# Performance work log

Measured on AMD Instinct MI355X. Metric: run time of the kernel, lower is better.

## Reference

```python
import jax, jax.numpy as jnp
import numpy as np
import math

N = 20000          # real nodes (batch_size)
D = 256            # hidden_dim
H = 4              # num_heads
L = 3              # num_layers
E = 320000         # local edges
EXP_DEG = 4        # expander_degree
LN_EPS = 1e-5


def setup_inputs() -> dict:
    key = jax.random.key(0)
    ks = jax.random.split(key, 8)
    x = jax.random.normal(ks[0], (N, D), jnp.float32)
    rng = np.random.default_rng(0)
    edge_index = jnp.asarray(rng.integers(0, N, size=(2, E)), dtype=jnp.int32)
    # Expander: EXP_DEG//2 random permutations on N+1 nodes (incl. virtual node),
    # each contributing edges in both directions -> degree-EXP_DEG regular graph.
    n = N + 1
    perms = [rng.permutation(n) for _ in range(EXP_DEG // 2)]
    src = np.concatenate([np.arange(n) for _ in perms] + perms)
    dst = np.concatenate(perms + [np.arange(n) for _ in perms])
    exp_edge_index = jnp.asarray(np.stack([src, dst]), dtype=jnp.int32)
    s_in = 1.0 / math.sqrt(D)
    s_ffn = 1.0 / math.sqrt(4 * D)
    def w(k, shape, s):
        return jax.random.normal(k, shape, jnp.float32) * s
    params = {
        'Wqkv_loc': w(ks[1], (L, D, 3 * D), s_in), 'bqkv_loc': jnp.zeros((L, 3 * D), jnp.float32),
        'Wo_loc':   w(ks[2], (L, D, D), s_in),     'bo_loc':   jnp.zeros((L, D), jnp.float32),
        'Wqkv_exp': w(ks[3], (L, D, 3 * D), s_in), 'bqkv_exp': jnp.zeros((L, 3 * D), jnp.float32),
        'Wo_exp':   w(ks[4], (L, D, D), s_in),     'bo_exp':   jnp.zeros((L, D), jnp.float32),
        'ln_g': jnp.ones((L, D), jnp.float32),     'ln_b': jnp.zeros((L, D), jnp.float32),
        'W1': w(ks[5], (L, D, 4 * D), s_in),       'b1': jnp.zeros((L, 4 * D), jnp.float32),
        'W2': w(ks[6], (L, 4 * D, D), s_ffn),      'b2': jnp.zeros((L, D), jnp.float32),
    }
    return {'x': x, 'edge_index': edge_index, 'exp_edge_index': exp_edge_index, **params}


def _attention(h, src, dst, Wqkv, bqkv, Wo, bo):
    # Sparse multi-head attention over (src -> dst) edges with segment softmax per dst.
    n, d = h.shape
    dh = d // H
    qkv = (h @ Wqkv + bqkv).reshape(n, 3, H, dh)
    q, k, v = qkv[:, 0], qkv[:, 1], qkv[:, 2]            # [n, H, dh]
    score = (q[dst] * k[src]).sum(-1) / jnp.sqrt(jnp.float32(dh))  # [e, H]
    m = jax.ops.segment_max(score, dst, num_segments=n)  # [n, H]
    ex = jnp.exp(score - m[dst])
    denom = jax.ops.segment_sum(ex, dst, num_segments=n)
    alpha = ex / (denom[dst] + 1e-16)
    out = jax.ops.segment_sum(alpha[:, :, None] * v[src], dst, num_segments=n)  # [n, H, dh]
    return out.reshape(n, d) @ Wo + bo


def _layer_norm(x, g, b):
    mu = x.mean(-1, keepdims=True)
    var = ((x - mu) ** 2).mean(-1, keepdims=True)
    return (x - mu) * jax.lax.rsqrt(var + LN_EPS) * g + b


def reference(x, edge_index, exp_edge_index, Wqkv_loc, bqkv_loc, Wo_loc, bo_loc,
              Wqkv_exp, bqkv_exp, Wo_exp, bo_exp, ln_g, ln_b, W1, b1, W2, b2):
    n0 = x.shape[0]
    # VirtualNode transform: append one zero-feature node connected to/from all nodes.
    h = jnp.concatenate([x, jnp.zeros((1, x.shape[1]), x.dtype)], axis=0)
    ar = jnp.arange(n0, dtype=edge_index.dtype)
    vn = jnp.full((n0,), n0, dtype=edge_index.dtype)
    src = jnp.concatenate([edge_index[0], ar, vn])
    dst = jnp.concatenate([edge_index[1], vn, ar])
    esrc, edst = exp_edge_index[0], exp_edge_index[1]
    for l in range(L):  # fixed small number of structurally distinct layers
        res = h
        loc = _attention(h, src, dst, Wqkv_loc[l], bqkv_loc[l], Wo_loc[l], bo_loc[l])
        exp = _attention(h, esrc, edst, Wqkv_exp[l], bqkv_exp[l], Wo_exp[l], bo_exp[l])
        h = _layer_norm(res + loc + exp, ln_g[l], ln_b[l])
        h = h + (jax.nn.gelu(h @ W1[l] + b1[l], approximate=False) @ W2[l] + b2[l])
    return h[:n0]
```

## Files before the change

kernel.cpp:

```cpp
#include <hip/hip_runtime.h>
#include <stdint.h>

#define NREAL   20000
#define NNODES  20001
#define VN      20000
#define E_EDGES 320000
#define NEXP    80004
#define MPAD    20096
#define NVNW    320

typedef unsigned short u16;
typedef unsigned int   u32;
typedef __bf16 bf16x8 __attribute__((ext_vector_type(8)));
typedef float  f32x4  __attribute__((ext_vector_type(4)));
typedef u16    u16x8  __attribute__((ext_vector_type(8)));

__device__ __host__ __forceinline__ size_t fmoff(int row, int col, int LD) {
    return (size_t)(row >> 4) * ((size_t)LD * 16) + (size_t)((col >> 3) * 128)
         + (size_t)((row & 15) * 8) + (size_t)(col & 7);
}

__device__ __forceinline__ int qkv_perm(int n) {
    if (n < 256) return n;
    int u = n - 256;
    int part = u >> 8;
    int cl = u & 255;
    return 256 + (cl >> 2) * 8 + part * 4 + (cl & 3);
}

__device__ __forceinline__ float bf2f(u16 v) {
    union { u32 u; float f; } x; x.u = ((u32)v) << 16; return x.f;
}
__device__ __forceinline__ u16 f2bf(float f) {
    union { float f; u32 u; } x; x.f = f;
    u32 r = (x.u + 0x7fffu + ((x.u >> 16) & 1u)) >> 16;
    return (u16)r;
}
__device__ __forceinline__ float4 cvt4(ushort4 u) {
    return make_float4(bf2f(u.x), bf2f(u.y), bf2f(u.z), bf2f(u.w));
}
__device__ __forceinline__ float4 ld4bf(const u16* p) { return cvt4(*(const ushort4*)p); }
__device__ __forceinline__ float4 cvtk8(u16x8 r) {
    return make_float4(bf2f(r[0]), bf2f(r[1]), bf2f(r[2]), bf2f(r[3]));
}
__device__ __forceinline__ float4 cvtv8(u16x8 r) {
    return make_float4(bf2f(r[4]), bf2f(r[5]), bf2f(r[6]), bf2f(r[7]));
}


__global__ void hinit_kernel(const float* __restrict__ x, float* __restrict__ h,
                             u16* __restrict__ hb) {
    int idx = blockIdx.x * 256 + threadIdx.x;
    if (idx >= NNODES * 64) return;
    int row = idx >> 6, c0 = (idx & 63) * 4;
    float4 v = make_float4(0.f, 0.f, 0.f, 0.f);
    if (row < NREAL) v = *(const float4*)(x + (size_t)row * 256 + c0);
    *(float4*)(h + (size_t)row * 256 + c0) = v;
    ushort4 o;
    o.x = f2bf(v.x); o.y = f2bf(v.y); o.z = f2bf(v.z); o.w = f2bf(v.w);
    *(ushort4*)(hb + fmoff(row, c0, 256)) = o;
}

__global__ void init_kernel(int* cnt, int* fill, int* ecnt,
                            const float* __restrict__ bl, const float* __restrict__ be,
                            float* __restrict__ bcat,
                            const float* __restrict__ bol, const float* __restrict__ boe,
                            float* __restrict__ bsum) {
    int i = blockIdx.x * 256 + threadIdx.x;
    if (i < NREAL) { cnt[i] = 0; fill[i] = 0; }
    if (i < NNODES) ecnt[i] = 0;
    if (i < 3 * 1536) {
        int l = i / 1536, c = i - l * 1536;
        float v = (c < 768) ? bl[l * 768 + c] : be[l * 768 + c - 768];
        int cc = (c >= 768) ? c - 768 : c;
        int d = qkv_perm(cc) + ((c >= 768) ? 768 : 0);
        bcat[l * 1536 + d] = v;
    }
    if (i < 3 * 256) bsum[i] = bol[i] + boe[i];
}

__global__ void csr_count_kernel(const int* __restrict__ ei, int* __restrict__ cnt) {
    int e = blockIdx.x * 256 + threadIdx.x;
    if (e < E_EDGES) atomicAdd(&cnt[ei[E_EDGES + e]], 1);
}

__global__ void csr_scan_kernel(const int* __restrict__ cnt, int* __restrict__ indptr) {
    __shared__ int ssum[256];
    int t = threadIdx.x;
    int c0 = t * 79;
    int s = 0;
    for (int j = 0; j < 79; j++) {
        int i = c0 + j;
        if (i < NREAL) s += cnt[i];
    }
    ssum[t] = s;
    __syncthreads();
    for (int d2 = 1; d2 < 256; d2 <<= 1) {
        int v = (t >= d2) ? ssum[t - d2] : 0;
        __syncthreads();
        ssum[t] += v;
        __syncthreads();
    }
    int run = (t == 0) ? 0 : ssum[t - 1];
    for (int j = 0; j < 79; j++) {
        int i = c0 + j;
        if (i < NREAL) { indptr[i] = run; run += cnt[i]; }
    }
    if (t == 255) indptr[NREAL] = run;
}

__global__ void csr_scatter_kernel(const int* __restrict__ ei, const int* __restrict__ indptr,
                                   int* __restrict__ fill, int* __restrict__ srcs) {
    int e = blockIdx.x * 256 + threadIdx.x;
    if (e < E_EDGES) {
        int d = ei[E_EDGES + e];
        int pos = indptr[d] + atomicAdd(&fill[d], 1);
        srcs[pos] = ei[e];
    }
}

__global__ void exp_scatter_kernel(const int* __restrict__ eei, int* __restrict__ ecnt,
                                   int* __restrict__ esrcs) {
    int e = blockIdx.x * 256 + threadIdx.x;
    if (e < NEXP) {
        int d = eei[NEXP + e];
        int pos = atomicAdd(&ecnt[d], 1);
        esrcs[d * 4 + pos] = eei[e];
    }
}

__global__ void wconv_all_kernel(const float* __restrict__ WqkvL, const float* __restrict__ WqkvE,
                                 const float* __restrict__ WoL, const float* __restrict__ WoE,
                                 const float* __restrict__ W1, const float* __restrict__ W2,
                                 u16* __restrict__ out) {
    int i = blockIdx.x * 256 + threadIdx.x;
    if (i >= 3 * 1048576) return;
    int l = i / 1048576, r = i - l * 1048576;
    if (r >= 393216 && r < 524288) {
        int r2 = r - 393216;
        int k = r2 >> 8, n = r2 & 255;
        float v = (k < 256) ? WoL[(size_t)l * 65536 + k * 256 + n]
                            : WoE[(size_t)l * 65536 + (k - 256) * 256 + n];
        out[(size_t)l * 1048576 + 393216 + fmoff(n, k, 512)] = f2bf(v);
        return;
    }
    const float* src; int K, N; int base;
    if (r < 196608)      { src = WqkvL; K = 256;  N = 768;  base = 0; }
    else if (r < 393216) { src = WqkvE; K = 256;  N = 768;  base = 196608; }
    else if (r < 786432) { src = W1;    K = 256;  N = 1024; base = 524288; }
    else                 { src = W2;    K = 1024; N = 256;  base = 786432; }
    int r2 = r - base;
    int k = r2 / N, n = r2 - k * N;
    int d = (r < 393216) ? qkv_perm(n) : n;
    out[(size_t)l * 1048576 + base + fmoff(d, k, K)] = f2bf(src[(size_t)l * K * N + r2]);
}

__global__ __launch_bounds__(256) void qkv_rw(
    const u16* __restrict__ A, const u16* __restrict__ Bt, const float* __restrict__ bias,
    u16* __restrict__ Q0, u16* __restrict__ KV0,
    u16* __restrict__ Q1, u16* __restrict__ KV1, int M) {
    const int lin = blockIdx.x;
    const int mt = lin / 6, ns = lin - mt * 6;
    const int tm = mt * 32;
    if (tm >= M) return;
    const int tid = threadIdx.x;
    const int w = tid >> 6, lane = tid & 63;
    const int lm = lane & 15, q = lane >> 4;

    f32x4 acc[2][4];
#pragma unroll
    for (int a = 0; a < 2; a++)
#pragma unroll
        for (int b = 0; b < 4; b++) acc[a][b] = (f32x4)0.0f;

    const u16* apf[2];
    const u16* bpf[4];
#pragma unroll
    for (int mi = 0; mi < 2; mi++)
        apf[mi] = A + (size_t)(tm / 16 + mi) * 4096 + q * 128 + lm * 8;
#pragma unroll
    for (int ni = 0; ni < 4; ni++)
        bpf[ni] = Bt + (size_t)(ns * 16 + w * 4 + ni) * 4096 + q * 128 + lm * 8;

    bf16x8 sA[4][2], sB[4][4];
#pragma unroll
    for (int s = 0; s < 3; s++) {
#pragma unroll
        for (int mi = 0; mi < 2; mi++) sA[s][mi] = *(const bf16x8*)(apf[mi] + s * 512);
#pragma unroll
        for (int ni = 0; ni < 4; ni++) sB[s][ni] = *(const bf16x8*)(bpf[ni] + s * 512);
    }
#pragma unroll
    for (int i = 0; i < 8; i++) {
        const int cu = i & 3, pf = (i + 3) & 3;
        if (i + 3 < 8) {
#pragma unroll
            for (int mi = 0; mi < 2; mi++) sA[pf][mi] = *(const bf16x8*)(apf[mi] + (i + 3) * 512);
#pragma unroll
            for (int ni = 0; ni < 4; ni++) sB[pf][ni] = *(const bf16x8*)(bpf[ni] + (i + 3) * 512);
        }
#pragma unroll
        for (int mi = 0; mi < 2; mi++)
#pragma unroll
            for (int ni = 0; ni < 4; ni++)
                acc[mi][ni] = __builtin_amdgcn_mfma_f32_16x16x32_bf16(
                    sB[cu][ni], sA[cu][mi], acc[mi][ni], 0, 0, 0);
    }

    float4 b4[4];
#pragma unroll
    for (int ni = 0; ni < 4; ni++)
        b4[ni] = *(const float4*)(bias + ns * 256 + w * 64 + ni * 16 + q * 4);

#pragma unroll
    for (int mi = 0; mi < 2; mi++) {
        int grow = tm + mi * 16 + lm;
        if (grow >= M) continue;
#pragma unroll
        for (int ni = 0; ni < 4; ni++) {
            int gcol = ns * 256 + w * 64 + ni * 16 + q * 4;
            float v0 = acc[mi][ni][0] + b4[ni].x;
            float v1 = acc[mi][ni][1] + b4[ni].y;
            float v2 = acc[mi][ni][2] + b4[ni].z;
            float v3 = acc[mi][ni][3] + b4[ni].w;
            ushort4 o;
            o.x = f2bf(v0); o.y = f2bf(v1); o.z = f2bf(v2); o.w = f2bf(v3);
            u16* dst;
            if (gcol < 256)       dst = Q0  + (size_t)grow * 256 + gcol;
            else if (gcol < 768)  dst = KV0 + (size_t)grow * 512 + (gcol - 256);
            else if (gcol < 1024) dst = Q1  + (size_t)grow * 256 + (gcol - 768);
            else                  dst = KV1 + (size_t)grow * 512 + (gcol - 1024);
            *(ushort4*)dst = o;
        }
    }
}

__global__ __launch_bounds__(256) void ffn1_rw(
    const u16* __restrict__ A, const u16* __restrict__ Bt, const float* __restrict__ bias,
    u16* __restrict__ Cb, int M) {
    const int lin = blockIdx.x;
    const int mt = lin >> 2, ns = lin & 3;
    const int tm = mt * 32;
    if (tm >= M) return;
    const int tid = threadIdx.x;
    const int w = tid >> 6, lane = tid & 63;
    const int lm = lane & 15, q = lane >> 4;

    f32x4 acc[2][4];
#pragma unroll
    for (int a = 0; a < 2; a++)
#pragma unroll
        for (int b = 0; b < 4; b++) acc[a][b] = (f32x4)0.0f;

    const u16* apf[2];
    const u16* bpf[4];
#pragma unroll
    for (int mi = 0; mi < 2; mi++)
        apf[mi] = A + (size_t)(tm / 16 + mi) * 4096 + q * 128 + lm * 8;
#pragma unroll
    for (int ni = 0; ni < 4; ni++)
        bpf[ni] = Bt + (size_t)(ns * 16 + w * 4 + ni) * 4096 + q * 128 + lm * 8;

    bf16x8 sA[4][2], sB[4][4];
#pragma unroll
    for (int s = 0; s < 3; s++) {
#pragma unroll
        for (int mi = 0; mi < 2; mi++) sA[s][mi] = *(const bf16x8*)(apf[mi] + s * 512);
#pragma unroll
        for (int ni = 0; ni < 4; ni++) sB[s][ni] = *(const bf16x8*)(bpf[ni] + s * 512);
    }
#pragma unroll
    for (int i = 0; i < 8; i++) {
        const int cu = i & 3, pf = (i + 3) & 3;
        if (i + 3 < 8) {
#pragma unroll
            for (int mi = 0; mi < 2; mi++) sA[pf][mi] = *(const bf16x8*)(apf[mi] + (i + 3) * 512);
#pragma unroll
            for (int ni = 0; ni < 4; ni++) sB[pf][ni] = *(const bf16x8*)(bpf[ni] + (i + 3) * 512);
        }
#pragma unroll
        for (int mi = 0; mi < 2; mi++)
#pragma unroll
            for (int ni = 0; ni < 4; ni++)
                acc[mi][ni] = __builtin_amdgcn_mfma_f32_16x16x32_bf16(
                    sB[cu][ni], sA[cu][mi], acc[mi][ni], 0, 0, 0);
    }

    float4 b4[4];
#pragma unroll
    for (int ni = 0; ni < 4; ni++)
        b4[ni] = *(const float4*)(bias + ns * 256 + w * 64 + ni * 16 + q * 4);

#pragma unroll
    for (int mi = 0; mi < 2; mi++) {
        int grow = tm + mi * 16 + lm;
        if (grow >= M) continue;
#pragma unroll
        for (int ni = 0; ni < 4; ni++) {
            int gcol = ns * 256 + w * 64 + ni * 16 + q * 4;
            float v0 = acc[mi][ni][0] + b4[ni].x;
            float v1 = acc[mi][ni][1] + b4[ni].y;
            float v2 = acc[mi][ni][2] + b4[ni].z;
            float v3 = acc[mi][ni][3] + b4[ni].w;
            float g0, g1, g2, g3;
            {
                float u = 0.7978845608f * (v0 + 0.044715f * v0 * v0 * v0);
                g0 = 0.5f * v0 * (2.0f - 2.0f / (__expf(2.0f * u) + 1.0f));
            }
            {
                float u = 0.7978845608f * (v1 + 0.044715f * v1 * v1 * v1);
                g1 = 0.5f * v1 * (2.0f - 2.0f / (__expf(2.0f * u) + 1.0f));
            }
            {
                float u = 0.7978845608f * (v2 + 0.044715f * v2 * v2 * v2);
                g2 = 0.5f * v2 * (2.0f - 2.0f / (__expf(2.0f * u) + 1.0f));
            }
            {
                float u = 0.7978845608f * (v3 + 0.044715f * v3 * v3 * v3);
                g3 = 0.5f * v3 * (2.0f - 2.0f / (__expf(2.0f * u) + 1.0f));
            }
            ushort4 o;
            o.x = f2bf(g0); o.y = f2bf(g1); o.z = f2bf(g2); o.w = f2bf(g3);
            *(ushort4*)(Cb + fmoff(grow, gcol, 1024)) = o;
        }
    }
}

__global__ __launch_bounds__(256) void wo_ln_rw(
    const u16* A, const u16* __restrict__ Bt, const float* __restrict__ bias,
    const float* __restrict__ resid, const float* __restrict__ g,
    const float* __restrict__ bvec, float* __restrict__ hout, u16* __restrict__ hb,
    const float* __restrict__ part, u16* acat_w, int M) {
    __shared__ float smS[32][4];
    __shared__ float smQ[32][4];
    const int tm = blockIdx.x * 32;
    if (tm >= M) return;
    const int tid = threadIdx.x;
    const int w = tid >> 6, lane = tid & 63;
    const int lm = lane & 15, q = lane >> 4;

    if (blockIdx.x == VN / 32) {
        __shared__ float smm[4][64][6];
        int hh = lane >> 4;
        int ov = (hh << 6) + (lane & 15) * 4;
        float mm = -1e30f, ll = 0.0f;
        float ax = 0, ay = 0, az = 0, aw = 0;
        for (int p = w * 80; p < w * 80 + 80; p++) {
            const float* pp = part + (size_t)p * 264;
            float pm = pp[hh], pl = pp[4 + hh];
            float4 nm = *(const float4*)(pp + 8 + ov);
            float Mn = fmaxf(mm, pm);
            float s0 = __expf(mm - Mn);
            float s1 = __expf(pm - Mn);
            ax = ax * s0 + nm.x * s1;
            ay = ay * s0 + nm.y * s1;
            az = az * s0 + nm.z * s1;
            aw = aw * s0 + nm.w * s1;
            ll = ll * s0 + pl * s1;
            mm = Mn;
        }
        smm[w][lane][0] = mm; smm[w][lane][1] = ll;
        smm[w][lane][2] = ax; smm[w][lane][3] = ay;
        smm[w][lane][4] = az; smm[w][lane][5] = aw;
        __syncthreads();
        if (w == 0) {
            float M2 = -1e30f, L2 = 0.0f;
            float bx = 0, by = 0, bz = 0, bw = 0;
#pragma unroll
            for (int p = 0; p < 4; p++) {
                float pm = smm[p][lane][0], pl = smm[p][lane][1];
                float Mn = fmaxf(M2, pm);
                float s0 = __expf(M2 - Mn);
                float s1 = __expf(pm - Mn);
                bx = bx * s0 + smm[p][lane][2] * s1;
                by = by * s0 + smm[p][lane][3] * s1;
                bz = bz * s0 + smm[p][lane][4] * s1;
                bw = bw * s0 + smm[p][lane][5] * s1;
                L2 = L2 * s0 + pl * s1;
                M2 = Mn;
            }
            float inv = 1.0f / (L2 + 1e-16f);
            ushort4 o;
            o.x = f2bf(bx * inv); o.y = f2bf(by * inv);
            o.z = f2bf(bz * inv); o.w = f2bf(bw * inv);
            *(ushort4*)(acat_w + fmoff(VN, ov, 512)) = o;
        }
        __syncthreads();
    }

    f32x4 acc[2][4];
#pragma unroll
    for (int a = 0; a < 2; a++)
#pragma unroll
        for (int b = 0; b < 4; b++) acc[a][b] = (f32x4)0.0f;

    const u16* apf[2];
    const u16* bpf[4];
#pragma unroll
    for (int mi = 0; mi < 2; mi++)
        apf[mi] = A + (size_t)(tm / 16 + mi) * 8192 + q * 128 + lm * 8;
#pragma unroll
    for (int ni = 0; ni < 4; ni++)
        bpf[ni] = Bt + (size_t)(w * 4 + ni) * 8192 + q * 128 + lm * 8;

    bf16x8 sA[4][2], sB[4][4];
#pragma unroll
    for (int s = 0; s < 3; s++) {
#pragma unroll
        for (int mi = 0; mi < 2; mi++) sA[s][mi] = *(const bf16x8*)(apf[mi] + s * 512);
#pragma unroll
        for (int ni = 0; ni < 4; ni++) sB[s][ni] = *(const bf16x8*)(bpf[ni] + s * 512);
    }
#pragma unroll
    for (int i = 0; i < 16; i++) {
        const int cu = i & 3, pf = (i + 3) & 3;
        if (i + 3 < 16) {
#pragma unroll
            for (int mi = 0; mi < 2; mi++) sA[pf][mi] = *(const bf16x8*)(apf[mi] + (i + 3) * 512);
#pragma unroll
            for (int ni = 0; ni < 4; ni++) sB[pf][ni] = *(const bf16x8*)(bpf[ni] + (i + 3) * 512);
        }
#pragma unroll
        for (int mi = 0; mi < 2; mi++)
#pragma unroll
            for (int ni = 0; ni < 4; ni++)
                acc[mi][ni] = __builtin_amdgcn_mfma_f32_16x16x32_bf16(
                    sB[cu][ni], sA[cu][mi], acc[mi][ni], 0, 0, 0);
    }

    float4 b4[4];
#pragma unroll
    for (int ni = 0; ni < 4; ni++)
        b4[ni] = *(const float4*)(bias + w * 64 + ni * 16 + q * 4);
#pragma unroll
    for (int mi = 0; mi < 2; mi++) {
        int grow = tm + mi * 16 + lm;
#pragma unroll
        for (int ni = 0; ni < 4; ni++) {
            int gcol = w * 64 + ni * 16 + q * 4;
            size_t idx = (size_t)grow * 256 + gcol;
            float4 rv = *(const float4*)(resid + idx);
            acc[mi][ni][0] = rv.x + (acc[mi][ni][0] + b4[ni].x);
            acc[mi][ni][1] = rv.y + (acc[mi][ni][1] + b4[ni].y);
            acc[mi][ni][2] = rv.z + (acc[mi][ni][2] + b4[ni].z);
            acc[mi][ni][3] = rv.w + (acc[mi][ni][3] + b4[ni].w);
        }
    }

    float s1[2];
#pragma unroll
    for (int mi = 0; mi < 2; mi++) {
        float s = 0.f;
#pragma unroll
        for (int ni = 0; ni < 4; ni++)
            s += acc[mi][ni][0] + acc[mi][ni][1] + acc[mi][ni][2] + acc[mi][ni][3];
        s += __shfl_xor(s, 16); s += __shfl_xor(s, 32);
        s1[mi] = s;
    }
    if (lane < 16) {
        smS[lm][w] = s1[0];
        smS[16 + lm][w] = s1[1];
    }
    __syncthreads();
    float mu[2];
#pragma unroll
    for (int mi = 0; mi < 2; mi++) {
        int r = mi * 16 + lm;
        mu[mi] = (smS[r][0] + smS[r][1] + smS[r][2] + smS[r][3]) * (1.0f / 256.0f);
    }
    float s2[2];
#pragma unroll
    for (int mi = 0; mi < 2; mi++) {
        float s = 0.f;
#pragma unroll
        for (int ni = 0; ni < 4; ni++) {
            float d0 = acc[mi][ni][0] - mu[mi];
            float d1 = acc[mi][ni][1] - mu[mi];
            float d2 = acc[mi][ni][2] - mu[mi];
            float d3 = acc[mi][ni][3] - mu[mi];
            s += d0 * d0 + d1 * d1 + d2 * d2 + d3 * d3;
        }
        s += __shfl_xor(s, 16); s += __shfl_xor(s, 32);
        s2[mi] = s;
    }
    if (lane < 16) {
        smQ[lm][w] = s2[0];
        smQ[16 + lm][w] = s2[1];
    }
    __syncthreads();
    float rinv[2];
#pragma unroll
    for (int mi = 0; mi < 2; mi++) {
        int r = mi * 16 + lm;
        float var = (smQ[r][0] + smQ[r][1] + smQ[r][2] + smQ[r][3]) * (1.0f / 256.0f);
        rinv[mi] = 1.0f / sqrtf(var + 1e-5f);
    }
#pragma unroll
    for (int mi = 0; mi < 2; mi++) {
        int grow = tm + mi * 16 + lm;
        if (grow >= M) continue;
#pragma unroll
        for (int ni = 0; ni < 4; ni++) {
            int gcol = w * 64 + ni * 16 + q * 4;
            float4 gv = *(const float4*)(g + gcol);
            float4 bv = *(const float4*)(bvec + gcol);
            float4 y;
            y.x = (acc[mi][ni][0] - mu[mi]) * rinv[mi] * gv.x + bv.x;
            y.y = (acc[mi][ni][1] - mu[mi]) * rinv[mi] * gv.y + bv.y;
            y.z = (acc[mi][ni][2] - mu[mi]) * rinv[mi] * gv.z + bv.z;
            y.w = (acc[mi][ni][3] - mu[mi]) * rinv[mi] * gv.w + bv.w;
            *(float4*)(hout + (size_t)grow * 256 + gcol) = y;
            ushort4 o;
            o.x = f2bf(y.x); o.y = f2bf(y.y); o.z = f2bf(y.z); o.w = f2bf(y.w);
            *(ushort4*)(hb + fmoff(grow, gcol, 256)) = o;
        }
    }
}

__global__ __launch_bounds__(256) void w2_rw(
    const u16* __restrict__ A, const u16* __restrict__ Bt, const float* __restrict__ bias,
    const float* __restrict__ resid, float* __restrict__ Cf, u16* __restrict__ Cb,
    int last, int M) {
    const int tm = blockIdx.x * 32;
    if (tm >= M) return;
    const int tid = threadIdx.x;
    const int w = tid >> 6, lane = tid & 63;
    const int lm = lane & 15, q = lane >> 4;

    f32x4 acc[2][4];
#pragma unroll
    for (int a = 0; a < 2; a++)
#pragma unroll
        for (int b = 0; b < 4; b++) acc[a][b] = (f32x4)0.0f;

    const u16* apf[2];
    const u16* bpf[4];
#pragma unroll
    for (int mi = 0; mi < 2; mi++)
        apf[mi] = A + (size_t)(tm / 16 + mi) * 16384 + q * 128 + lm * 8;
#pragma unroll
    for (int ni = 0; ni < 4; ni++)
        bpf[ni] = Bt + (size_t)(w * 4 + ni) * 16384 + q * 128 + lm * 8;

    bf16x8 sA[4][2], sB[4][4];
#pragma unroll
    for (int s = 0; s < 3; s++) {
#pragma unroll
        for (int mi = 0; mi < 2; mi++) sA[s][mi] = *(const bf16x8*)(apf[mi] + s * 512);
#pragma unroll
        for (int ni = 0; ni < 4; ni++) sB[s][ni] = *(const bf16x8*)(bpf[ni] + s * 512);
    }
#pragma unroll
    for (int i = 0; i < 32; i++) {
        const int cu = i & 3, pf = (i + 3) & 3;
        if (i + 3 < 32) {
#pragma unroll
            for (int mi = 0; mi < 2; mi++) sA[pf][mi] = *(const bf16x8*)(apf[mi] + (i + 3) * 512);
#pragma unroll
            for (int ni = 0; ni < 4; ni++) sB[pf][ni] = *(const bf16x8*)(bpf[ni] + (i + 3) * 512);
        }
#pragma unroll
        for (int mi = 0; mi < 2; mi++)
#pragma unroll
            for (int ni = 0; ni < 4; ni++)
                acc[mi][ni] = __builtin_amdgcn_mfma_f32_16x16x32_bf16(
                    sB[cu][ni], sA[cu][mi], acc[mi][ni], 0, 0, 0);
    }

    float4 b4[4];
#pragma unroll
    for (int ni = 0; ni < 4; ni++)
        b4[ni] = *(const float4*)(bias + w * 64 + ni * 16 + q * 4);

#pragma unroll
    for (int mi = 0; mi < 2; mi++) {
        int grow = tm + mi * 16 + lm;
        if (grow >= (last ? NREAL : M)) continue;
#pragma unroll
        for (int ni = 0; ni < 4; ni++) {
            int gcol = w * 64 + ni * 16 + q * 4;
            float v0 = acc[mi][ni][0] + b4[ni].x;
            float v1 = acc[mi][ni][1] + b4[ni].y;
            float v2 = acc[mi][ni][2] + b4[ni].z;
            float v3 = acc[mi][ni][3] + b4[ni].w;
            size_t idx = (size_t)grow * 256 + gcol;
            float4 rv = *(const float4*)(resid + idx);
            float o0 = rv.x + v0, o1 = rv.y + v1, o2 = rv.z + v2, o3 = rv.w + v3;
            *(float4*)(Cf + idx) = make_float4(o0, o1, o2, o3);
            if (!last) {
                ushort4 o;
                o.x = f2bf(o0); o.y = f2bf(o1); o.z = f2bf(o2); o.w = f2bf(o3);
                *(ushort4*)(Cb + fmoff(grow, gcol, 256)) = o;
            }
        }
    }
}

__global__ void attn_fused_kernel(const u16* __restrict__ qb_loc, const u16* __restrict__ kv_loc,
                                  const u16* __restrict__ qb_exp, const u16* __restrict__ kv_exp,
                                  const int* __restrict__ indptr, const int* __restrict__ srcs,
                                  const int* __restrict__ esrcs,
                                  u16* __restrict__ acat, float* __restrict__ part) {
    int gw0 = (int)((blockIdx.x * (size_t)blockDim.x + threadIdx.x) >> 6);
    int gw = __builtin_amdgcn_readfirstlane(gw0);
    int lane = threadIdx.x & 63;
    int h = lane >> 4;
    int off = (h << 6) + (lane & 15) * 4;
    int coff = (off >> 2) * 8;

    if (gw < NVNW) {
        int wv = gw;
        float4 qv = ld4bf(qb_loc + (size_t)VN * 256 + off);
        float m = -1e30f, l = 0.0f;
        float ax = 0, ay = 0, az = 0, aw = 0;
        for (int i = wv; i < NREAL; i += NVNW) {
            u16x8 r = *(const u16x8*)(kv_loc + (size_t)i * 512 + coff);
            float4 k4 = cvtk8(r);
            float4 v4 = cvtv8(r);
            float s = qv.x * k4.x + qv.y * k4.y + qv.z * k4.z + qv.w * k4.w;
            s += __shfl_xor(s, 1); s += __shfl_xor(s, 2);
            s += __shfl_xor(s, 4); s += __shfl_xor(s, 8);
            float sc = s * 0.125f;
            float mn = fmaxf(m, sc);
            float fold = __expf(m - mn);
            float ee = __expf(sc - mn);
            ax = ax * fold + v4.x * ee;
            ay = ay * fold + v4.y * ee;
            az = az * fold + v4.z * ee;
            aw = aw * fold + v4.w * ee;
            l = l * fold + ee;
            m = mn;
        }
        float* pp = part + (size_t)wv * 264;
        if ((lane & 15) == 0) { pp[h] = m; pp[4 + h] = l; }
        *(float4*)(pp + 8 + off) = make_float4(ax, ay, az, aw);
        return;
    }
    gw -= NVNW;

    const u16 *qb, *kv;
    const int* sl;
    int node, beg, deg, tot, cbase;
    if (gw < NREAL) {
        node = gw; qb = qb_loc; kv = kv_loc; sl = srcs; cbase = 0;
        beg = indptr[node]; deg = indptr[node + 1] - beg; tot = deg + 1;
    } else if (gw < NREAL + NNODES) {
        node = gw - NREAL;
        qb = qb_exp; kv = kv_exp; sl = esrcs; cbase = 256;
        beg = node * 4; deg = 4; tot = 4;
    } else {
        return;
    }

    float4 qv = ld4bf(qb + (size_t)node * 256 + off);
    float m = -1e30f, l = 0.0f;
    float ax = 0, ay = 0, az = 0, aw = 0;

    if (tot <= 4) {
        u16x8 raw[4];
#pragma unroll
        for (int j = 0; j < 4; j++) {
            int s = (j < deg) ? sl[beg + j] : VN;
            raw[j] = *(const u16x8*)(kv + (size_t)s * 512 + coff);
        }
        float sc[4];
#pragma unroll
        for (int j = 0; j < 4; j++) {
            float4 k4 = cvtk8(raw[j]);
            float p = qv.x * k4.x + qv.y * k4.y + qv.z * k4.z + qv.w * k4.w;
            p += __shfl_xor(p, 1); p += __shfl_xor(p, 2);
            p += __shfl_xor(p, 4); p += __shfl_xor(p, 8);
            sc[j] = (j < tot) ? p * 0.125f : -1e30f;
        }
        float mn = fmaxf(fmaxf(sc[0], sc[1]), fmaxf(sc[2], sc[3]));
#pragma unroll
        for (int j = 0; j < 4; j++) {
            float ee = __expf(sc[j] - mn);
            float4 v4 = cvtv8(raw[j]);
            ax += v4.x * ee; ay += v4.y * ee; az += v4.z * ee; aw += v4.w * ee;
            l += ee;
        }
        m = mn;
    } else {
        const int nch = (tot + 7) >> 3;
        u16x8 rA[8], rB[8];
#pragma unroll
        for (int j = 0; j < 8; j++) {
            int s = (j < deg) ? sl[beg + j] : VN;
            rA[j] = *(const u16x8*)(kv + (size_t)s * 512 + coff);
        }
        for (int c = 0; c < nch; c++) {
            if (c + 1 < nch) {
                const int e0n = (c + 1) * 8;
#pragma unroll
                for (int j = 0; j < 8; j++) {
                    int e = e0n + j;
                    int s = (e < deg) ? sl[beg + e] : VN;
                    rB[j] = *(const u16x8*)(kv + (size_t)s * 512 + coff);
                }
            }
            const int e0 = c * 8;
            float sc[8];
#pragma unroll
            for (int j = 0; j < 8; j++) {
                float4 k4 = cvtk8(rA[j]);
                float p = qv.x * k4.x + qv.y * k4.y + qv.z * k4.z + qv.w * k4.w;
                p += __shfl_xor(p, 1); p += __shfl_xor(p, 2);
                p += __shfl_xor(p, 4); p += __shfl_xor(p, 8);
                sc[j] = (e0 + j < tot) ? p * 0.125f : -1e30f;
            }
            float cmax = fmaxf(fmaxf(fmaxf(sc[0], sc[1]), fmaxf(sc[2], sc[3])),
                               fmaxf(fmaxf(sc[4], sc[5]), fmaxf(sc[6], sc[7])));
            float mn = fmaxf(m, cmax);
            float fold = __expf(m - mn);
            ax *= fold; ay *= fold; az *= fold; aw *= fold; l *= fold;
#pragma unroll
            for (int j = 0; j < 8; j++) {
                float ee = __expf(sc[j] - mn);
                float4 v4 = cvtv8(rA[j]);
                ax += v4.x * ee; ay += v4.y * ee; az += v4.z * ee; aw += v4.w * ee;
                l += ee;
            }
            m = mn;
#pragma unroll
            for (int j = 0; j < 8; j++) rA[j] = rB[j];
        }
    }
    float inv = 1.0f / (l + 1e-16f);
    ushort4 o;
    o.x = f2bf(ax * inv); o.y = f2bf(ay * inv);
    o.z = f2bf(az * inv); o.w = f2bf(aw * inv);
    *(ushort4*)(acat + fmoff(node, cbase + off, 512)) = o;
}


extern "C" void kernel_launch(void* const* d_in, const int* in_sizes, int n_in,
                              void* d_out, int out_size, void* d_ws, size_t ws_size,
                              hipStream_t stream) {
    (void)in_sizes; (void)n_in; (void)out_size;
    const float* x        = (const float*)d_in[0];
    const int*   ei       = (const int*)d_in[1];
    const int*   eei      = (const int*)d_in[2];
    const float* Wqkv_loc = (const float*)d_in[3];
    const float* bqkv_loc = (const float*)d_in[4];
    const float* Wo_loc   = (const float*)d_in[5];
    const float* bo_loc   = (const float*)d_in[6];
    const float* Wqkv_exp = (const float*)d_in[7];
    const float* bqkv_exp = (const float*)d_in[8];
    const float* Wo_exp   = (const float*)d_in[9];
    const float* bo_exp   = (const float*)d_in[10];
    const float* ln_g     = (const float*)d_in[11];
    const float* ln_b     = (const float*)d_in[12];
    const float* W1       = (const float*)d_in[13];
    const float* b1       = (const float*)d_in[14];
    const float* W2       = (const float*)d_in[15];
    const float* b2       = (const float*)d_in[16];

    char* wsp = (char*)d_ws;
    size_t off = 0;
    auto carve = [&](size_t bytes) -> void* {
        void* p = wsp + off;
        off += (bytes + 255) & ~(size_t)255;
        return p;
    };
    float* h_f    = (float*)carve((size_t)NNODES * 256 * 4);
    u16*   h_b    = (u16*)carve((size_t)MPAD * 256 * 2);
    u16*   qb_loc = (u16*)carve((size_t)NNODES * 256 * 2);
    u16*   kv_loc = (u16*)carve((size_t)NNODES * 512 * 2);
    u16*   qb_exp = (u16*)carve((size_t)NNODES * 256 * 2);
    u16*   kv_exp = (u16*)carve((size_t)NNODES * 512 * 2);
    u16*   acat   = (u16*)carve((size_t)MPAD * 512 * 2);
    u16*   wbf    = (u16*)carve((size_t)3 * 1048576 * 2);
    float* bcat   = (float*)carve((size_t)3 * 1536 * 4);
    float* bsum   = (float*)carve((size_t)3 * 256 * 4);
    int*   cnt    = (int*)carve((size_t)NREAL * 4);
    int*   indptr = (int*)carve((size_t)(NREAL + 1) * 4);
    int*   fill   = (int*)carve((size_t)NREAL * 4);
    int*   srcs   = (int*)carve((size_t)E_EDGES * 4);
    int*   ecnt   = (int*)carve((size_t)NNODES * 4);
    int*   esrcs  = (int*)carve((size_t)NNODES * 4 * 4);
    float* part   = (float*)carve((size_t)NVNW * 264 * 4);
    u16*   mid_d  = (u16*)carve((size_t)MPAD * 1024 * 2);
    u16*   mid    = (ws_size >= off) ? mid_d : qb_loc;

    hinit_kernel<<<(NNODES * 64 + 255) / 256, 256, 0, stream>>>(x, h_f, h_b);
    init_kernel<<<(NNODES + 255) / 256, 256, 0, stream>>>(
        cnt, fill, ecnt, bqkv_loc, bqkv_exp, bcat, bo_loc, bo_exp, bsum);
    csr_count_kernel<<<(E_EDGES + 255) / 256, 256, 0, stream>>>(ei, cnt);
    csr_scan_kernel<<<1, 256, 0, stream>>>(cnt, indptr);
    csr_scatter_kernel<<<(E_EDGES + 255) / 256, 256, 0, stream>>>(ei, indptr, fill, srcs);
    exp_scatter_kernel<<<(NEXP + 255) / 256, 256, 0, stream>>>(eei, ecnt, esrcs);
    wconv_all_kernel<<<(3 * 1048576 + 255) / 256, 256, 0, stream>>>(
        Wqkv_loc, Wqkv_exp, Wo_loc, Wo_exp, W1, W2, wbf);

    const int ATTN_BLOCKS = (NVNW + NREAL + NNODES + 3) / 4;
    const int RW32_BLOCKS = MPAD / 32;
    const int QKV_BLOCKS  = RW32_BLOCKS * 6;
    const int FFN1_BLOCKS = RW32_BLOCKS * 4;

    for (int l = 0; l < 3; l++) {
        const u16* wqkvC = wbf + (size_t)l * 1048576 + 0;
        const u16* wocat = wbf + (size_t)l * 1048576 + 393216;
        const u16* w1T   = wbf + (size_t)l * 1048576 + 524288;
        const u16* w2T   = wbf + (size_t)l * 1048576 + 786432;

        qkv_rw<<<QKV_BLOCKS, 256, 0, stream>>>(
            h_b, wqkvC, bcat + l * 1536,
            qb_loc, kv_loc, qb_exp, kv_exp, NNODES);

        attn_fused_kernel<<<ATTN_BLOCKS, 256, 0, stream>>>(
            qb_loc, kv_loc, qb_exp, kv_exp, indptr, srcs, esrcs, acat, part);

        wo_ln_rw<<<RW32_BLOCKS, 256, 0, stream>>>(
            acat, wocat, bsum + l * 256, h_f,
            ln_g + l * 256, ln_b + l * 256, h_f, h_b, part, acat, NNODES);

        ffn1_rw<<<FFN1_BLOCKS, 256, 0, stream>>>(
            h_b, w1T, b1 + l * 1024, mid, NNODES);

        if (l < 2) {
            w2_rw<<<RW32_BLOCKS, 256, 0, stream>>>(
                mid, w2T, b2 + l * 256, h_f, h_f, h_b, 0, NNODES);
        } else {
            w2_rw<<<RW32_BLOCKS, 256, 0, stream>>>(
                mid, w2T, b2 + l * 256, h_f, (float*)d_out, nullptr, 1, NNODES);
        }
    }
}
```

Baseline: 766.4 us.

## Fuse FFN up-projection, GELU and down-projection into one kernel

Merges the W1+GELU kernel and the W2+residual kernel into a single kernel per 32-row tile. The 1024-wide GELU intermediate is produced in four 256-column chunks, each staged in LDS and immediately consumed by the W2 accumulation. This removes the global write and read of the bf16 intermediate buffer and one launch per layer. In exchange, the grid for the first GEMM shrinks to a quarter as many blocks, two block-wide barriers are added per chunk, and the register prefetch depth drops from three stages to two.

```diff
diff --git a/kernel.cpp b/kernel.cpp
--- a/kernel.cpp
+++ b/kernel.cpp
@@ -235,93 +235,168 @@
     }
 }
 
-__global__ __launch_bounds__(256) void ffn1_rw(
-    const u16* __restrict__ A, const u16* __restrict__ Bt, const float* __restrict__ bias,
-    u16* __restrict__ Cb, int M) {
-    const int lin = blockIdx.x;
-    const int mt = lin >> 2, ns = lin & 3;
-    const int tm = mt * 32;
+__global__ __launch_bounds__(256) void ffn_fused(
+    const u16* __restrict__ A, const u16* __restrict__ W1t, const u16* __restrict__ W2t,
+    const float* __restrict__ b1v, const float* __restrict__ b2v,
+    const float* __restrict__ resid, float* __restrict__ Cf, u16* __restrict__ Cb,
+    int last, int M) {
+    __shared__ u16 smid[32 * 256];
+    const int tm = blockIdx.x * 32;
     if (tm >= M) return;
     const int tid = threadIdx.x;
     const int w = tid >> 6, lane = tid & 63;
     const int lm = lane & 15, q = lane >> 4;
 
-    f32x4 acc[2][4];
+    f32x4 acc2[2][4];
 #pragma unroll
     for (int a = 0; a < 2; a++)
 #pragma unroll
-        for (int b = 0; b < 4; b++) acc[a][b] = (f32x4)0.0f;
+        for (int b = 0; b < 4; b++) acc2[a][b] = (f32x4)0.0f;
 
     const u16* apf[2];
-    const u16* bpf[4];
 #pragma unroll
     for (int mi = 0; mi < 2; mi++)
         apf[mi] = A + (size_t)(tm / 16 + mi) * 4096 + q * 128 + lm * 8;
+    const u16* bpf2[4];
 #pragma unroll
     for (int ni = 0; ni < 4; ni++)
-        bpf[ni] = Bt + (size_t)(ns * 16 + w * 4 + ni) * 4096 + q * 128 + lm * 8;
-
-    bf16x8 sA[4][2], sB[4][4];
-#pragma unroll
-    for (int s = 0; s < 3; s++) {
-#pragma unroll
-        for (int mi = 0; mi < 2; mi++) sA[s][mi] = *(const bf16x8*)(apf[mi] + s * 512);
-#pragma unroll
-        for (int ni = 0; ni < 4; ni++) sB[s][ni] = *(const bf16x8*)(bpf[ni] + s * 512);
-    }
-#pragma unroll
-    for (int i = 0; i < 8; i++) {
-        const int cu = i & 3, pf = (i + 3) & 3;
-        if (i + 3 < 8) {
-#pragma unroll
-            for (int mi = 0; mi < 2; mi++) sA[pf][mi] = *(const bf16x8*)(apf[mi] + (i + 3) * 512);
-#pragma unroll
-            for (int ni = 0; ni < 4; ni++) sB[pf][ni] = *(const bf16x8*)(bpf[ni] + (i + 3) * 512);
-        }
-#pragma unroll
-        for (int mi = 0; mi < 2; mi++)
-#pragma unroll
-            for (int ni = 0; ni < 4; ni++)
-                acc[mi][ni] = __builtin_amdgcn_mfma_f32_16x16x32_bf16(
-                    sB[cu][ni], sA[cu][mi], acc[mi][ni], 0, 0, 0);
-    }
-
-    float4 b4[4];
+        bpf2[ni] = W2t + (size_t)(w * 4 + ni) * 16384 + q * 128 + lm * 8;
+    const u16* alds[2];
+#pragma unroll
+    for (int mi = 0; mi < 2; mi++)
+        alds[mi] = smid + mi * 4096 + q * 128 + lm * 8;
+
+    for (int c = 0; c < 4; c++) {
+        f32x4 acc1[2][4];
+#pragma unroll
+        for (int a = 0; a < 2; a++)
+#pragma unroll
+            for (int b = 0; b < 4; b++) acc1[a][b] = (f32x4)0.0f;
+        const u16* bpf1[4];
+#pragma unroll
+        for (int ni = 0; ni < 4; ni++)
+            bpf1[ni] = W1t + (size_t)(c * 16 + w * 4 + ni) * 4096 + q * 128 + lm * 8;
+
+        {
+            bf16x8 sA[3][2], sB[3][4];
+#pragma unroll
+            for (int s = 0; s < 2; s++) {
+#pragma unroll
+                for (int mi = 0; mi < 2; mi++) sA[s][mi] = *(const bf16x8*)(apf[mi] + s * 512);
+#pragma unroll
+                for (int ni = 0; ni < 4; ni++) sB[s][ni] = *(const bf16x8*)(bpf1[ni] + s * 512);
+            }
+#pragma unroll
+            for (int i = 0; i < 8; i++) {
+                const int cu = i % 3, pf = (i + 2) % 3;
+                if (i + 2 < 8) {
+#pragma unroll
+                    for (int mi = 0; mi < 2; mi++)
+                        sA[pf][mi] = *(const bf16x8*)(apf[mi] + (i + 2) * 512);
+#pragma unroll
+                    for (int ni = 0; ni < 4; ni++)
+                        sB[pf][ni] = *(const bf16x8*)(bpf1[ni] + (i + 2) * 512);
+                }
+#pragma unroll
+                for (int mi = 0; mi < 2; mi++)
+#pragma unroll
+                    for (int ni = 0; ni < 4; ni++)
+                        acc1[mi][ni] = __builtin_amdgcn_mfma_f32_16x16x32_bf16(
+                            sB[cu][ni], sA[cu][mi], acc1[mi][ni], 0, 0, 0);
+            }
+        }
+        float4 b4[4];
+#pragma unroll
+        for (int ni = 0; ni < 4; ni++)
+            b4[ni] = *(const float4*)(b1v + c * 256 + w * 64 + ni * 16 + q * 4);
+#pragma unroll
+        for (int mi = 0; mi < 2; mi++) {
+#pragma unroll
+            for (int ni = 0; ni < 4; ni++) {
+                int lrow = mi * 16 + lm;
+                int lcol = w * 64 + ni * 16 + q * 4;
+                float v0 = acc1[mi][ni][0] + b4[ni].x;
+                float v1 = acc1[mi][ni][1] + b4[ni].y;
+                float v2 = acc1[mi][ni][2] + b4[ni].z;
+                float v3 = acc1[mi][ni][3] + b4[ni].w;
+                float g0, g1, g2, g3;
+                {
+                    float u = 0.7978845608f * (v0 + 0.044715f * v0 * v0 * v0);
+                    g0 = 0.5f * v0 * (2.0f - 2.0f / (__expf(2.0f * u) + 1.0f));
+                }
+                {
+                    float u = 0.7978845608f * (v1 + 0.044715f * v1 * v1 * v1);
+                    g1 = 0.5f * v1 * (2.0f - 2.0f / (__expf(2.0f * u) + 1.0f));
+                }
+                {
+                    float u = 0.7978845608f * (v2 + 0.044715f * v2 * v2 * v2);
+                    g2 = 0.5f * v2 * (2.0f - 2.0f / (__expf(2.0f * u) + 1.0f));
+                }
+                {
+                    float u = 0.7978845608f * (v3 + 0.044715f * v3 * v3 * v3);
+                    g3 = 0.5f * v3 * (2.0f - 2.0f / (__expf(2.0f * u) + 1.0f));
+                }
+                ushort4 o;
+                o.x = f2bf(g0); o.y = f2bf(g1); o.z = f2bf(g2); o.w = f2bf(g3);
+                *(ushort4*)(smid + fmoff(lrow, lcol, 256)) = o;
+            }
+        }
+        __syncthreads();
+
+        {
+            bf16x8 tB[3][4];
+#pragma unroll
+            for (int s = 0; s < 2; s++)
+#pragma unroll
+                for (int ni = 0; ni < 4; ni++)
+                    tB[s][ni] = *(const bf16x8*)(bpf2[ni] + (c * 8 + s) * 512);
+#pragma unroll
+            for (int i = 0; i < 8; i++) {
+                const int cu = i % 3, pf = (i + 2) % 3;
+                if (i + 2 < 8) {
+#pragma unroll
+                    for (int ni = 0; ni < 4; ni++)
+                        tB[pf][ni] = *(const bf16x8*)(bpf2[ni] + (c * 8 + i + 2) * 512);
+                }
+                bf16x8 a0 = *(const bf16x8*)(alds[0] + i * 512);
+                bf16x8 a1 = *(const bf16x8*)(alds[1] + i * 512);
+#pragma unroll
+                for (int ni = 0; ni < 4; ni++) {
+                    acc2[0][ni] = __builtin_amdgcn_mfma_f32_16x16x32_bf16(
+                        tB[cu][ni], a0, acc2[0][ni], 0, 0, 0);
+                    acc2[1][ni] = __builtin_amdgcn_mfma_f32_16x16x32_bf16(
+                        tB[cu][ni], a1, acc2[1][ni], 0, 0, 0);
+                }
+            }
+        }
+        __syncthreads();
+    }
+
+    float4 c4[4];
 #pragma unroll
     for (int ni = 0; ni < 4; ni++)
-        b4[ni] = *(const float4*)(bias + ns * 256 + w * 64 + ni * 16 + q * 4);
+        c4[ni] = *(const float4*)(b2v + w * 64 + ni * 16 + q * 4);
 
 #pragma unroll
     for (int mi = 0; mi < 2; mi++) {
         int grow = tm + mi * 16 + lm;
-        if (grow >= M) continue;
+        if (grow >= (last ? NREAL : M)) continue;
 #pragma unroll
         for (int ni = 0; ni < 4; ni++) {
-            int gcol = ns * 256 + w * 64 + ni * 16 + q * 4;
-            float v0 = acc[mi][ni][0] + b4[ni].x;
-            float v1 = acc[mi][ni][1] + b4[ni].y;
-            float v2 = acc[mi][ni][2] + b4[ni].z;
-            float v3 = acc[mi][ni][3] + b4[ni].w;
-            float g0, g1, g2, g3;
-            {
-                float u = 0.7978845608f * (v0 + 0.044715f * v0 * v0 * v0);
-                g0 = 0.5f * v0 * (2.0f - 2.0f / (__expf(2.0f * u) + 1.0f));
+            int gcol = w * 64 + ni * 16 + q * 4;
+            float v0 = acc2[mi][ni][0] + c4[ni].x;
+            float v1 = acc2[mi][ni][1] + c4[ni].y;
+            float v2 = acc2[mi][ni][2] + c4[ni].z;
+            float v3 = acc2[mi][ni][3] + c4[ni].w;
+            size_t idx = (size_t)grow * 256 + gcol;
+            float4 rv = *(const float4*)(resid + idx);
+            float o0 = rv.x + v0, o1 = rv.y + v1, o2 = rv.z + v2, o3 = rv.w + v3;
+            *(float4*)(Cf + idx) = make_float4(o0, o1, o2, o3);
+            if (!last) {
+                ushort4 o;
+                o.x = f2bf(o0); o.y = f2bf(o1); o.z = f2bf(o2); o.w = f2bf(o3);
+                *(ushort4*)(Cb + fmoff(grow, gcol, 256)) = o;
             }
-            {
-                float u = 0.7978845608f * (v1 + 0.044715f * v1 * v1 * v1);
-                g1 = 0.5f * v1 * (2.0f - 2.0f / (__expf(2.0f * u) + 1.0f));
-            }
-            {
-                float u = 0.7978845608f * (v2 + 0.044715f * v2 * v2 * v2);
-                g2 = 0.5f * v2 * (2.0f - 2.0f / (__expf(2.0f * u) + 1.0f));
-            }
-            {
-                float u = 0.7978845608f * (v3 + 0.044715f * v3 * v3 * v3);
-                g3 = 0.5f * v3 * (2.0f - 2.0f / (__expf(2.0f * u) + 1.0f));
-            }
-            ushort4 o;
-            o.x = f2bf(g0); o.y = f2bf(g1); o.z = f2bf(g2); o.w = f2bf(g3);
-            *(ushort4*)(Cb + fmoff(grow, gcol, 1024)) = o;
         }
     }
 }
@@ -513,85 +588,6 @@
             ushort4 o;
             o.x = f2bf(y.x); o.y = f2bf(y.y); o.z = f2bf(y.z); o.w = f2bf(y.w);
             *(ushort4*)(hb + fmoff(grow, gcol, 256)) = o;
-        }
-    }
-}
-
-__global__ __launch_bounds__(256) void w2_rw(
-    const u16* __restrict__ A, const u16* __restrict__ Bt, const float* __restrict__ bias,
-    const float* __restrict__ resid, float* __restrict__ Cf, u16* __restrict__ Cb,
-    int last, int M) {
-    const int tm = blockIdx.x * 32;
-    if (tm >= M) return;
-    const int tid = threadIdx.x;
-    const int w = tid >> 6, lane = tid & 63;
-    const int lm = lane & 15, q = lane >> 4;
-
-    f32x4 acc[2][4];
-#pragma unroll
-    for (int a = 0; a < 2; a++)
-#pragma unroll
-        for (int b = 0; b < 4; b++) acc[a][b] = (f32x4)0.0f;
-
-    const u16* apf[2];
-    const u16* bpf[4];
-#pragma unroll
-    for (int mi = 0; mi < 2; mi++)
-        apf[mi] = A + (size_t)(tm / 16 + mi) * 16384 + q * 128 + lm * 8;
-#pragma unroll
-    for (int ni = 0; ni < 4; ni++)
-        bpf[ni] = Bt + (size_t)(w * 4 + ni) * 16384 + q * 128 + lm * 8;
-
-    bf16x8 sA[4][2], sB[4][4];
-#pragma unroll
-    for (int s = 0; s < 3; s++) {
-#pragma unroll
-        for (int mi = 0; mi < 2; mi++) sA[s][mi] = *(const bf16x8*)(apf[mi] + s * 512);
-#pragma unroll
-        for (int ni = 0; ni < 4; ni++) sB[s][ni] = *(const bf16x8*)(bpf[ni] + s * 512);
-    }
-#pragma unroll
-    for (int i = 0; i < 32; i++) {
-        const int cu = i & 3, pf = (i + 3) & 3;
-        if (i + 3 < 32) {
-#pragma unroll
-            for (int mi = 0; mi < 2; mi++) sA[pf][mi] = *(const bf16x8*)(apf[mi] + (i + 3) * 512);
-#pragma unroll
-            for (int ni = 0; ni < 4; ni++) sB[pf][ni] = *(const bf16x8*)(bpf[ni] + (i + 3) * 512);
-        }
-#pragma unroll
-        for (int mi = 0; mi < 2; mi++)
-#pragma unroll
-            for (int ni = 0; ni < 4; ni++)
-                acc[mi][ni] = __builtin_amdgcn_mfma_f32_16x16x32_bf16(
-                    sB[cu][ni], sA[cu][mi], acc[mi][ni], 0, 0, 0);
-    }
-
-    float4 b4[4];
-#pragma unroll
-    for (int ni = 0; ni < 4; ni++)
-        b4[ni] = *(const float4*)(bias + w * 64 + ni * 16 + q * 4);
-
-#pragma unroll
-    for (int mi = 0; mi < 2; mi++) {
-        int grow = tm + mi * 16 + lm;
-        if (grow >= (last ? NREAL : M)) continue;
-#pragma unroll
-        for (int ni = 0; ni < 4; ni++) {
-            int gcol = w * 64 + ni * 16 + q * 4;
-            float v0 = acc[mi][ni][0] + b4[ni].x;
-            float v1 = acc[mi][ni][1] + b4[ni].y;
-            float v2 = acc[mi][ni][2] + b4[ni].z;
-            float v3 = acc[mi][ni][3] + b4[ni].w;
-            size_t idx = (size_t)grow * 256 + gcol;
-            float4 rv = *(const float4*)(resid + idx);
-            float o0 = rv.x + v0, o1 = rv.y + v1, o2 = rv.z + v2, o3 = rv.w + v3;
-            *(float4*)(Cf + idx) = make_float4(o0, o1, o2, o3);
-            if (!last) {
-                ushort4 o;
-                o.x = f2bf(o0); o.y = f2bf(o1); o.z = f2bf(o2); o.w = f2bf(o3);
-                *(ushort4*)(Cb + fmoff(grow, gcol, 256)) = o;
-            }
         }
     }
 }
@@ -737,7 +733,7 @@
 extern "C" void kernel_launch(void* const* d_in, const int* in_sizes, int n_in,
                               void* d_out, int out_size, void* d_ws, size_t ws_size,
                               hipStream_t stream) {
-    (void)in_sizes; (void)n_in; (void)out_size;
+    (void)in_sizes; (void)n_in; (void)out_size; (void)ws_size;
     const float* x        = (const float*)d_in[0];
     const int*   ei       = (const int*)d_in[1];
     const int*   eei      = (const int*)d_in[2];
@@ -780,8 +776,6 @@
     int*   ecnt   = (int*)carve((size_t)NNODES * 4);
     int*   esrcs  = (int*)carve((size_t)NNODES * 4 * 4);
     float* part   = (float*)carve((size_t)NVNW * 264 * 4);
-    u16*   mid_d  = (u16*)carve((size_t)MPAD * 1024 * 2);
-    u16*   mid    = (ws_size >= off) ? mid_d : qb_loc;
 
     hinit_kernel<<<(NNODES * 64 + 255) / 256, 256, 0, stream>>>(x, h_f, h_b);
     init_kernel<<<(NNODES + 255) / 256, 256, 0, stream>>>(
@@ -796,7 +790,6 @@
     const int ATTN_BLOCKS = (NVNW + NREAL + NNODES + 3) / 4;
     const int RW32_BLOCKS = MPAD / 32;
     const int QKV_BLOCKS  = RW32_BLOCKS * 6;
-    const int FFN1_BLOCKS = RW32_BLOCKS * 4;
 
     for (int l = 0; l < 3; l++) {
         const u16* wqkvC = wbf + (size_t)l * 1048576 + 0;
@@ -815,15 +808,14 @@
             acat, wocat, bsum + l * 256, h_f,
             ln_g + l * 256, ln_b + l * 256, h_f, h_b, part, acat, NNODES);
 
-        ffn1_rw<<<FFN1_BLOCKS, 256, 0, stream>>>(
-            h_b, w1T, b1 + l * 1024, mid, NNODES);
-
         if (l < 2) {
-            w2_rw<<<RW32_BLOCKS, 256, 0, stream>>>(
-                mid, w2T, b2 + l * 256, h_f, h_f, h_b, 0, NNODES);
+            ffn_fused<<<RW32_BLOCKS, 256, 0, stream>>>(
+                h_b, w1T, w2T, b1 + l * 1024, b2 + l * 256,
+                h_f, h_f, h_b, 0, NNODES);
         } else {
-            w2_rw<<<RW32_BLOCKS, 256, 0, stream>>>(
-                mid, w2T, b2 + l * 256, h_f, (float*)d_out, nullptr, 1, NNODES);
-        }
-    }
-}
+            ffn_fused<<<RW32_BLOCKS, 256, 0, stream>>>(
+                h_b, w1T, w2T, b1 + l * 1024, b2 + l * 256,
+                h_f, (float*)d_out, nullptr, 1, NNODES);
+        }
+    }
+}
```

Result: slower. 833.9 us (+8.8%).
